# Performance work log

Hardware: AMD Instinct MI355X
Metric: run time of the kernel (lower is better)

## Reference

```python
import jax, jax.numpy as jnp
import numpy as np
from jax import lax

SEQ, BATCH, IN, HID, OUT = 28, 8192, 28, 128, 10


def _lstm_layer(x, W_ih, W_hh, b_ih, b_hh):
    # x: [T, B, in]; PyTorch gate order: i, f, g, o
    # precompute input projection once (keeps scan body memory-bound on h only)
    xproj = jnp.einsum('tbi,gi->tbg', x, W_ih) + b_ih + b_hh  # [T, B, 4H]
    H = W_hh.shape[1]
    B = x.shape[1]
    h0 = jnp.zeros((B, H), x.dtype)
    c0 = jnp.zeros((B, H), x.dtype)

    def step(carry, xp_t):
        h, c = carry
        gates = xp_t + h @ W_hh.T  # [B, 4H]
        i, f, g, o = jnp.split(gates, 4, axis=-1)
        i = jax.nn.sigmoid(i)
        f = jax.nn.sigmoid(f)
        g = jnp.tanh(g)
        o = jax.nn.sigmoid(o)
        c = f * c + i * g
        h = o * jnp.tanh(c)
        return (h, c), h

    _, ys = lax.scan(step, (h0, c0), xproj)
    return ys  # [T, B, H]


def setup_inputs() -> dict:
    key = jax.random.key(0)
    ks = jax.random.split(key, 11)
    s_in = 1.0 / np.sqrt(HID)
    u = lambda k, shape: jax.random.uniform(k, shape, jnp.float32, -s_in, s_in)
    return {
        'X': jax.random.normal(ks[0], (SEQ, BATCH, IN), jnp.float32),
        'W_ih0': u(ks[1], (4 * HID, IN)),
        'W_hh0': u(ks[2], (4 * HID, HID)),
        'b_ih0': u(ks[3], (4 * HID,)),
        'b_hh0': u(ks[4], (4 * HID,)),
        'W_ih1': u(ks[5], (4 * HID, HID)),
        'W_hh1': u(ks[6], (4 * HID, HID)),
        'b_ih1': u(ks[7], (4 * HID,)),
        'b_hh1': u(ks[8], (4 * HID,)),
        'W_lin': u(ks[9], (OUT, HID)),
        'b_lin': u(ks[10], (OUT,)),
    }


def reference(X, W_ih0, W_hh0, b_ih0, b_hh0, W_ih1, W_hh1, b_ih1, b_hh1, W_lin, b_lin):
    h1 = _lstm_layer(X, W_ih0, W_hh0, b_ih0, b_hh0)   # [T, B, 128]
    h2 = _lstm_layer(h1, W_ih1, W_hh1, b_ih1, b_hh1)  # [T, B, 128]
    pred = h2[-1] @ W_lin.T + b_lin                   # [B, 10]
    return pred
```

## Files before the change

kernel.cpp:

```cpp
#include <hip/hip_runtime.h>
#include <hip/hip_bf16.h>

#define SEQ   28
#define BATCH 8192
#define NIN   28
#define HID   128
#define NOUT  10

#define SCL_SIG  (-1.4426950408889634f)
#define SCL_TANH (2.8853900817779268f)

typedef __bf16 bf16_t;
typedef __bf16 bf16x8 __attribute__((ext_vector_type(8)));
typedef float  f32x4  __attribute__((ext_vector_type(4)));

__device__ __forceinline__ unsigned swz(unsigned row, unsigned byte_in_row) {
    return row * 256u + (byte_in_row ^ ((row & 7u) << 4));
}

__device__ __forceinline__ void barrier_lds() {
    asm volatile("s_waitcnt lgkmcnt(0)\n\ts_barrier" ::: "memory");
}

__global__ void pack_w_kernel(const float* __restrict__ Whh0, bf16_t* __restrict__ o0,
                              const float* __restrict__ Whh1, bf16_t* __restrict__ o1,
                              const float* __restrict__ Wih1, bf16_t* __restrict__ o2) {
    int idx = blockIdx.x * 256 + threadIdx.x;
    int mi = idx >> 16;
    int e  = idx & 65535;
    const float* W = (mi == 0) ? Whh0 : (mi == 1) ? Whh1 : Wih1;
    bf16_t*      o = (mi == 0) ? o0   : (mi == 1) ? o1   : o2;
    int j    = e & 7;
    int frag = e >> 3;
    int lane = frag & 63;
    int ksnt = frag >> 6;
    int nt = ksnt & 31, ks = ksnt >> 5;
    int gate = nt * 16 + (lane & 15);
    int k    = ks * 32 + ((lane >> 4) << 3) + j;
    float s  = ((gate >> 7) == 2) ? SCL_TANH : SCL_SIG;
    o[e] = (bf16_t)(W[gate * 128 + k] * s);
}

__device__ __forceinline__ bf16x8 load_x0(const float* __restrict__ X,
                                          int t, int rb, int m, int l15, int l4) {
    const float* base = X + ((size_t)(t * BATCH + rb + 16 * m + l15)) * NIN + l4 * 8;
    f32x4 lo = *(const f32x4*)base;
    f32x4 hi = {0.f, 0.f, 0.f, 0.f};
    if (l4 < 3) hi = *(const f32x4*)(base + 4);
    bf16x8 v;
    #pragma unroll
    for (int j = 0; j < 4; ++j) { v[j] = (bf16_t)lo[j]; v[4 + j] = (bf16_t)hi[j]; }
    return v;
}

template <int LAYER>
__device__ __forceinline__ void lstm_step(
    int t, int tload, int rb, int tid, int lane, int w, int l15, int l4,
    unsigned char* smem,
    const float* __restrict__ X, const bf16_t* __restrict__ h1r,
    bf16_t* __restrict__ h1w,
    bf16x8 (&whh)[4][4], bf16x8 (&wih)[4][4],
    float (&bias)[4], float (&c)[2][4],
    bf16x8 (&xc)[4][2], bf16x8 (&xl)[4][2])
{
    constexpr int KS = (LAYER == 0) ? 1 : 4;
    unsigned char* hb = smem + ((t & 1) << 13);
    unsigned char* hn = smem + ((~t & 1) << 13);

    bf16x8 ah[4][2];
    #pragma unroll
    for (int ks = 0; ks < 4; ++ks)
        #pragma unroll
        for (int m = 0; m < 2; ++m)
            ah[ks][m] = *(const bf16x8*)(hb + swz(16 * m + l15, (ks * 32 + l4 * 8) * 2));

    f32x4 acc[2][4];
    #pragma unroll
    for (int m = 0; m < 2; ++m)
        #pragma unroll
        for (int q = 0; q < 4; ++q) {
            f32x4 b = {bias[q], bias[q], bias[q], bias[q]};
            acc[m][q] = b;
        }

    #pragma unroll
    for (int m = 0; m < 2; ++m)
        #pragma unroll
        for (int q = 0; q < 4; ++q)
            #pragma unroll
            for (int ks = 0; ks < KS; ++ks)
                acc[m][q] = __builtin_amdgcn_mfma_f32_16x16x32_bf16(
                    xc[ks][m], wih[q][ks], acc[m][q], 0, 0, 0);

    if (tload < SEQ) {
        if constexpr (LAYER == 0) {
            #pragma unroll
            for (int m = 0; m < 2; ++m)
                xl[0][m] = load_x0(X, tload, rb, m, l15, l4);
        } else {
            #pragma unroll
            for (int ks = 0; ks < 4; ++ks)
                #pragma unroll
                for (int m = 0; m < 2; ++m)
                    xl[ks][m] = *(const bf16x8*)(h1r + ((size_t)(tload * BATCH + rb + 16 * m + l15)) * HID + ks * 32 + l4 * 8);
        }
    }

    #pragma unroll
    for (int m = 0; m < 2; ++m)
        #pragma unroll
        for (int q = 0; q < 4; ++q)
            #pragma unroll
            for (int ks = 0; ks < 4; ++ks)
                acc[m][q] = __builtin_amdgcn_mfma_f32_16x16x32_bf16(
                    ah[ks][m], whh[q][ks], acc[m][q], 0, 0, 0);

    #pragma unroll
    for (int m = 0; m < 2; ++m)
        #pragma unroll
        for (int r = 0; r < 4; ++r) {
            float Ei = __builtin_amdgcn_exp2f(acc[m][0][r]);
            float Ef = __builtin_amdgcn_exp2f(acc[m][1][r]);
            float Eg = __builtin_amdgcn_exp2f(acc[m][2][r]);
            float Eo = __builtin_amdgcn_exp2f(acc[m][3][r]);
            float ti = 1.0f + Ei, tf = 1.0f + Ef;
            float tg = 1.0f + Eg, to = 1.0f + Eo;
            float titg = ti * tg;
            float num  = fmaf(c[m][r], titg, tf * (tg - 2.0f));
            float cn   = num * __builtin_amdgcn_rcpf(tf * titg);
            c[m][r] = cn;
            float Ec = __builtin_amdgcn_exp2f(SCL_TANH * cn);
            float hv = (Ec - 1.0f) * __builtin_amdgcn_rcpf(to * (1.0f + Ec));
            *(bf16_t*)(hn + swz(16 * m + l4 * 4 + r, (16 * w + l15) * 2)) = (bf16_t)hv;
        }
    barrier_lds();

    if constexpr (LAYER == 0) {
        int row = tid >> 4, sc = tid & 15;
        f32x4 v = *(const f32x4*)(hn + swz(row, sc * 16));
        *(f32x4*)((unsigned char*)h1w + ((size_t)(t * BATCH + rb + row)) * 256 + sc * 16) = v;
    }
}

__global__ __launch_bounds__(512, 2)
void lstm_fused_kernel(const float* __restrict__ Wih0,
                       const float* __restrict__ bih0, const float* __restrict__ bhh0,
                       const float* __restrict__ bih1, const float* __restrict__ bhh1,
                       const float* __restrict__ X,
                       const bf16_t* __restrict__ whhp0,
                       const bf16_t* __restrict__ whhp1,
                       const bf16_t* __restrict__ wihp1,
                       bf16_t* __restrict__ h1,
                       const float* __restrict__ Wlin, const float* __restrict__ blin,
                       float* __restrict__ out)
{
    __shared__ unsigned char smem[16384] __attribute__((aligned(16)));

    const int tid  = threadIdx.x;
    const int lane = tid & 63;
    const int w    = tid >> 6;
    const int l15  = lane & 15;
    const int l4   = lane >> 4;
    const int rb   = blockIdx.x * 32;

    bf16x8 whh[4][4], wih[4][4];
    float  bias[4];
    float  c[2][4];
    bf16x8 xA[4][2], xB[4][2];

    #pragma unroll
    for (int q = 0; q < 4; ++q)
        #pragma unroll
        for (int ks = 0; ks < 4; ++ks)
            whh[q][ks] = *(const bf16x8*)(whhp0 + ((size_t)((ks * 32 + (w + 8 * q)) * 64 + lane)) * 8);
    #pragma unroll
    for (int q = 0; q < 4; ++q) {
        int gate = 16 * w + 128 * q + l15;
        float s = (q == 2) ? SCL_TANH : SCL_SIG;
        #pragma unroll
        for (int j = 0; j < 8; ++j) {
            int k = l4 * 8 + j;
            wih[q][0][j] = (k < NIN) ? (bf16_t)(Wih0[gate * NIN + k] * s) : (bf16_t)0.0f;
        }
        bias[q] = (bih0[gate] + bhh0[gate]) * s;
        c[0][q] = 0.f; c[1][q] = 0.f;
    }
    for (int i = tid * 16; i < 16384; i += 512 * 16) {
        f32x4 z = {0.f, 0.f, 0.f, 0.f};
        *(f32x4*)(smem + i) = z;
    }
    #pragma unroll
    for (int m = 0; m < 2; ++m) {
        xA[0][m] = load_x0(X, 0, rb, m, l15, l4);
        xB[0][m] = load_x0(X, 1, rb, m, l15, l4);
    }
    __syncthreads();

    for (int t = 0; t < SEQ; t += 2) {
        lstm_step<0>(t,     t + 2, rb, tid, lane, w, l15, l4, smem, X, nullptr, h1,
                     whh, wih, bias, c, xA, xA);
        lstm_step<0>(t + 1, t + 3, rb, tid, lane, w, l15, l4, smem, X, nullptr, h1,
                     whh, wih, bias, c, xB, xB);
    }

    __syncthreads();

    #pragma unroll
    for (int q = 0; q < 4; ++q) {
        #pragma unroll
        for (int ks = 0; ks < 4; ++ks) {
            whh[q][ks] = *(const bf16x8*)(whhp1 + ((size_t)((ks * 32 + (w + 8 * q)) * 64 + lane)) * 8);
            wih[q][ks] = *(const bf16x8*)(wihp1 + ((size_t)((ks * 32 + (w + 8 * q)) * 64 + lane)) * 8);
        }
        int gate = 16 * w + 128 * q + l15;
        float s = (q == 2) ? SCL_TANH : SCL_SIG;
        bias[q] = (bih1[gate] + bhh1[gate]) * s;
        c[0][q] = 0.f; c[1][q] = 0.f;
    }
    for (int i = tid * 16; i < 16384; i += 512 * 16) {
        f32x4 z = {0.f, 0.f, 0.f, 0.f};
        *(f32x4*)(smem + i) = z;
    }
    #pragma unroll
    for (int ks = 0; ks < 4; ++ks)
        #pragma unroll
        for (int m = 0; m < 2; ++m)
            xA[ks][m] = *(const bf16x8*)(h1 + ((size_t)(rb + 16 * m + l15)) * HID + ks * 32 + l4 * 8);
    __syncthreads();

    for (int t = 0; t < SEQ; ++t)
        lstm_step<1>(t, t + 1, rb, tid, lane, w, l15, l4, smem, nullptr, h1, nullptr,
                     whh, wih, bias, c, xA, xA);

    if (tid < 32 * NOUT) {
        int row = tid / NOUT, oc = tid % NOUT;
        const unsigned char* hf = smem;
        float s = blin[oc];
        #pragma unroll 8
        for (int k = 0; k < HID; ++k) {
            float h = (float)*(const bf16_t*)(hf + swz(row, k * 2));
            s += h * Wlin[oc * HID + k];
        }
        out[(size_t)(rb + row) * NOUT + oc] = s;
    }
}

extern "C" void kernel_launch(void* const* d_in, const int* in_sizes, int n_in,
                              void* d_out, int out_size, void* d_ws, size_t ws_size,
                              hipStream_t stream) {
    const float* X    = (const float*)d_in[0];
    const float* Wih0 = (const float*)d_in[1];
    const float* Whh0 = (const float*)d_in[2];
    const float* bih0 = (const float*)d_in[3];
    const float* bhh0 = (const float*)d_in[4];
    const float* Wih1 = (const float*)d_in[5];
    const float* Whh1 = (const float*)d_in[6];
    const float* bih1 = (const float*)d_in[7];
    const float* bhh1 = (const float*)d_in[8];
    const float* Wlin = (const float*)d_in[9];
    const float* blin = (const float*)d_in[10];
    float* out = (float*)d_out;

    unsigned char* ws = (unsigned char*)d_ws;
    bf16_t* h1    = (bf16_t*)(ws);
    bf16_t* whhp0 = (bf16_t*)(ws + 58720256);
    bf16_t* whhp1 = (bf16_t*)(ws + 58851328);
    bf16_t* wihp1 = (bf16_t*)(ws + 58982400);

    pack_w_kernel<<<dim3(768), dim3(256), 0, stream>>>(Whh0, whhp0, Whh1, whhp1, Wih1, wihp1);

    lstm_fused_kernel<<<dim3(256), dim3(512), 0, stream>>>(
        Wih0, bih0, bhh0, bih1, bhh1, X, whhp0, whhp1, wihp1, h1,
        Wlin, blin, out);
}
```

Before: 133.1 us.

## Software-pipeline LSTM steps: precompute next input projection during current step

Restructures each recurrent step so the input-projection MFMAs for the next timestep run after the current step's gate math, double-buffering accumulators across steps. The barrier moves to the start of each step and the h1 global writeback is deferred by one step, so the recurrent critical path holds only the h@W_hh MFMAs and the activations. The aim is to overlap independent input-projection work with the serial recurrence. The cost is more live registers (two accumulator sets), which may pressure occupancy at launch bounds (512,2).

```diff
diff --git a/kernel.cpp b/kernel.cpp
--- a/kernel.cpp
+++ b/kernel.cpp
@@ -54,75 +54,57 @@
 }
 
 template <int LAYER>
-__device__ __forceinline__ void lstm_step(
-    int t, int tload, int rb, int tid, int lane, int w, int l15, int l4,
+__device__ __forceinline__ void step_v2(
+    int t, int rb, int tid, int w, int l15, int l4,
     unsigned char* smem,
     const float* __restrict__ X, const bf16_t* __restrict__ h1r,
     bf16_t* __restrict__ h1w,
     bf16x8 (&whh)[4][4], bf16x8 (&wih)[4][4],
     float (&bias)[4], float (&c)[2][4],
-    bf16x8 (&xc)[4][2], bf16x8 (&xl)[4][2])
+    bf16x8 (&x)[4][2],
+    f32x4 (&accIn)[2][4], f32x4 (&accOut)[2][4])
 {
     constexpr int KS = (LAYER == 0) ? 1 : 4;
-    unsigned char* hb = smem + ((t & 1) << 13);
-    unsigned char* hn = smem + ((~t & 1) << 13);
-
-    bf16x8 ah[4][2];
-    #pragma unroll
-    for (int ks = 0; ks < 4; ++ks)
+    unsigned char* hb = smem + ((~t & 1) << 13);
+    unsigned char* hn = smem + ((t & 1) << 13);
+
+    barrier_lds();
+
+    if constexpr (LAYER == 0) {
+        if (t >= 1) {
+            int row = tid >> 4, sc = tid & 15;
+            f32x4 v = *(const f32x4*)(hb + swz(row, sc * 16));
+            *(f32x4*)((unsigned char*)h1w + ((size_t)((t - 1) * BATCH + rb + row)) * 256 + sc * 16) = v;
+        }
+    }
+
+    #pragma unroll
+    for (int kc = 0; kc < 2; ++kc) {
+        bf16x8 a0[2], a1[2];
+        #pragma unroll
+        for (int m = 0; m < 2; ++m) {
+            a0[m] = *(const bf16x8*)(hb + swz(16 * m + l15, ((2 * kc) * 32 + l4 * 8) * 2));
+            a1[m] = *(const bf16x8*)(hb + swz(16 * m + l15, ((2 * kc + 1) * 32 + l4 * 8) * 2));
+        }
         #pragma unroll
         for (int m = 0; m < 2; ++m)
-            ah[ks][m] = *(const bf16x8*)(hb + swz(16 * m + l15, (ks * 32 + l4 * 8) * 2));
-
-    f32x4 acc[2][4];
-    #pragma unroll
-    for (int m = 0; m < 2; ++m)
-        #pragma unroll
-        for (int q = 0; q < 4; ++q) {
-            f32x4 b = {bias[q], bias[q], bias[q], bias[q]};
-            acc[m][q] = b;
-        }
-
-    #pragma unroll
-    for (int m = 0; m < 2; ++m)
-        #pragma unroll
-        for (int q = 0; q < 4; ++q)
-            #pragma unroll
-            for (int ks = 0; ks < KS; ++ks)
-                acc[m][q] = __builtin_amdgcn_mfma_f32_16x16x32_bf16(
-                    xc[ks][m], wih[q][ks], acc[m][q], 0, 0, 0);
-
-    if (tload < SEQ) {
-        if constexpr (LAYER == 0) {
-            #pragma unroll
-            for (int m = 0; m < 2; ++m)
-                xl[0][m] = load_x0(X, tload, rb, m, l15, l4);
-        } else {
-            #pragma unroll
-            for (int ks = 0; ks < 4; ++ks)
-                #pragma unroll
-                for (int m = 0; m < 2; ++m)
-                    xl[ks][m] = *(const bf16x8*)(h1r + ((size_t)(tload * BATCH + rb + 16 * m + l15)) * HID + ks * 32 + l4 * 8);
-        }
-    }
-
-    #pragma unroll
-    for (int m = 0; m < 2; ++m)
-        #pragma unroll
-        for (int q = 0; q < 4; ++q)
-            #pragma unroll
-            for (int ks = 0; ks < 4; ++ks)
-                acc[m][q] = __builtin_amdgcn_mfma_f32_16x16x32_bf16(
-                    ah[ks][m], whh[q][ks], acc[m][q], 0, 0, 0);
-
-    #pragma unroll
-    for (int m = 0; m < 2; ++m)
+            #pragma unroll
+            for (int q = 0; q < 4; ++q) {
+                accIn[m][q] = __builtin_amdgcn_mfma_f32_16x16x32_bf16(
+                    a0[m], whh[q][2 * kc], accIn[m][q], 0, 0, 0);
+                accIn[m][q] = __builtin_amdgcn_mfma_f32_16x16x32_bf16(
+                    a1[m], whh[q][2 * kc + 1], accIn[m][q], 0, 0, 0);
+            }
+    }
+
+    #pragma unroll
+    for (int m = 0; m < 2; ++m) {
         #pragma unroll
         for (int r = 0; r < 4; ++r) {
-            float Ei = __builtin_amdgcn_exp2f(acc[m][0][r]);
-            float Ef = __builtin_amdgcn_exp2f(acc[m][1][r]);
-            float Eg = __builtin_amdgcn_exp2f(acc[m][2][r]);
-            float Eo = __builtin_amdgcn_exp2f(acc[m][3][r]);
+            float Ei = __builtin_amdgcn_exp2f(accIn[m][0][r]);
+            float Ef = __builtin_amdgcn_exp2f(accIn[m][1][r]);
+            float Eg = __builtin_amdgcn_exp2f(accIn[m][2][r]);
+            float Eo = __builtin_amdgcn_exp2f(accIn[m][3][r]);
             float ti = 1.0f + Ei, tf = 1.0f + Ef;
             float tg = 1.0f + Eg, to = 1.0f + Eo;
             float titg = ti * tg;
@@ -133,12 +115,29 @@
             float hv = (Ec - 1.0f) * __builtin_amdgcn_rcpf(to * (1.0f + Ec));
             *(bf16_t*)(hn + swz(16 * m + l4 * 4 + r, (16 * w + l15) * 2)) = (bf16_t)hv;
         }
-    barrier_lds();
-
-    if constexpr (LAYER == 0) {
-        int row = tid >> 4, sc = tid & 15;
-        f32x4 v = *(const f32x4*)(hn + swz(row, sc * 16));
-        *(f32x4*)((unsigned char*)h1w + ((size_t)(t * BATCH + rb + row)) * 256 + sc * 16) = v;
+        #pragma unroll
+        for (int q = 0; q < 4; ++q) {
+            f32x4 b = {bias[q], bias[q], bias[q], bias[q]};
+            accOut[m][q] = b;
+            #pragma unroll
+            for (int ks = 0; ks < KS; ++ks)
+                accOut[m][q] = __builtin_amdgcn_mfma_f32_16x16x32_bf16(
+                    x[ks][m], wih[q][ks], accOut[m][q], 0, 0, 0);
+        }
+    }
+
+    if (t + 2 < SEQ) {
+        if constexpr (LAYER == 0) {
+            #pragma unroll
+            for (int m = 0; m < 2; ++m)
+                x[0][m] = load_x0(X, t + 2, rb, m, l15, l4);
+        } else {
+            #pragma unroll
+            for (int ks = 0; ks < 4; ++ks)
+                #pragma unroll
+                for (int m = 0; m < 2; ++m)
+                    x[ks][m] = *(const bf16x8*)(h1r + ((size_t)((t + 2) * BATCH + rb + 16 * m + l15)) * HID + ks * 32 + l4 * 8);
+        }
     }
 }
 
@@ -166,7 +165,8 @@
     bf16x8 whh[4][4], wih[4][4];
     float  bias[4];
     float  c[2][4];
-    bf16x8 xA[4][2], xB[4][2];
+    bf16x8 x[4][2];
+    f32x4  accA[2][4], accB[2][4];
 
     #pragma unroll
     for (int q = 0; q < 4; ++q)
@@ -190,19 +190,33 @@
         *(f32x4*)(smem + i) = z;
     }
     #pragma unroll
-    for (int m = 0; m < 2; ++m) {
-        xA[0][m] = load_x0(X, 0, rb, m, l15, l4);
-        xB[0][m] = load_x0(X, 1, rb, m, l15, l4);
-    }
-    __syncthreads();
+    for (int m = 0; m < 2; ++m)
+        x[0][m] = load_x0(X, 0, rb, m, l15, l4);
+    #pragma unroll
+    for (int m = 0; m < 2; ++m)
+        #pragma unroll
+        for (int q = 0; q < 4; ++q) {
+            f32x4 b = {bias[q], bias[q], bias[q], bias[q]};
+            accA[m][q] = __builtin_amdgcn_mfma_f32_16x16x32_bf16(
+                x[0][m], wih[q][0], b, 0, 0, 0);
+        }
+    #pragma unroll
+    for (int m = 0; m < 2; ++m)
+        x[0][m] = load_x0(X, 1, rb, m, l15, l4);
 
     for (int t = 0; t < SEQ; t += 2) {
-        lstm_step<0>(t,     t + 2, rb, tid, lane, w, l15, l4, smem, X, nullptr, h1,
-                     whh, wih, bias, c, xA, xA);
-        lstm_step<0>(t + 1, t + 3, rb, tid, lane, w, l15, l4, smem, X, nullptr, h1,
-                     whh, wih, bias, c, xB, xB);
-    }
-
+        step_v2<0>(t,     rb, tid, w, l15, l4, smem, X, nullptr, h1,
+                   whh, wih, bias, c, x, accA, accB);
+        step_v2<0>(t + 1, rb, tid, w, l15, l4, smem, X, nullptr, h1,
+                   whh, wih, bias, c, x, accB, accA);
+    }
+
+    barrier_lds();
+    {
+        int row = tid >> 4, sc = tid & 15;
+        f32x4 v = *(const f32x4*)(smem + 8192 + swz(row, sc * 16));
+        *(f32x4*)((unsigned char*)h1 + ((size_t)(27 * BATCH + rb + row)) * 256 + sc * 16) = v;
+    }
     __syncthreads();
 
     #pragma unroll
@@ -225,16 +239,35 @@
     for (int ks = 0; ks < 4; ++ks)
         #pragma unroll
         for (int m = 0; m < 2; ++m)
-            xA[ks][m] = *(const bf16x8*)(h1 + ((size_t)(rb + 16 * m + l15)) * HID + ks * 32 + l4 * 8);
-    __syncthreads();
-
-    for (int t = 0; t < SEQ; ++t)
-        lstm_step<1>(t, t + 1, rb, tid, lane, w, l15, l4, smem, nullptr, h1, nullptr,
-                     whh, wih, bias, c, xA, xA);
+            x[ks][m] = *(const bf16x8*)(h1 + ((size_t)(rb + 16 * m + l15)) * HID + ks * 32 + l4 * 8);
+    #pragma unroll
+    for (int m = 0; m < 2; ++m)
+        #pragma unroll
+        for (int q = 0; q < 4; ++q) {
+            f32x4 b = {bias[q], bias[q], bias[q], bias[q]};
+            accA[m][q] = b;
+            #pragma unroll
+            for (int ks = 0; ks < 4; ++ks)
+                accA[m][q] = __builtin_amdgcn_mfma_f32_16x16x32_bf16(
+                    x[ks][m], wih[q][ks], accA[m][q], 0, 0, 0);
+        }
+    #pragma unroll
+    for (int ks = 0; ks < 4; ++ks)
+        #pragma unroll
+        for (int m = 0; m < 2; ++m)
+            x[ks][m] = *(const bf16x8*)(h1 + ((size_t)(BATCH + rb + 16 * m + l15)) * HID + ks * 32 + l4 * 8);
+
+    for (int t = 0; t < SEQ; t += 2) {
+        step_v2<1>(t,     rb, tid, w, l15, l4, smem, nullptr, h1, nullptr,
+                   whh, wih, bias, c, x, accA, accB);
+        step_v2<1>(t + 1, rb, tid, w, l15, l4, smem, nullptr, h1, nullptr,
+                   whh, wih, bias, c, x, accB, accA);
+    }
+    barrier_lds();
 
     if (tid < 32 * NOUT) {
         int row = tid / NOUT, oc = tid % NOUT;
-        const unsigned char* hf = smem;
+        const unsigned char* hf = smem + 8192;
         float s = blin[oc];
         #pragma unroll 8
         for (int k = 0; k < HID; ++k) {
```

After: 120.6 us. 1.1x faster.

## Software-pipeline LSTM steps by splitting batch tile into two interleaved halves

Applied to the files above, without the earlier changes.

The step is split into two half-steps over the two 16-row M tiles. The gate activations of one half are interleaved with the recurrent MFMAs of the other half, so transcendental math overlaps matrix work instead of running after it. The input projection for the next step is also issued early, and the h1 writeback is restructured per half. The cost is two barriers per timestep instead of one, plus more complex buffer parity logic with separate prologue and epilogue code.

```diff
diff --git a/kernel.cpp b/kernel.cpp
--- a/kernel.cpp
+++ b/kernel.cpp
@@ -13,6 +13,7 @@
 typedef __bf16 bf16_t;
 typedef __bf16 bf16x8 __attribute__((ext_vector_type(8)));
 typedef float  f32x4  __attribute__((ext_vector_type(4)));
+typedef float  f32x2  __attribute__((ext_vector_type(2)));
 
 __device__ __forceinline__ unsigned swz(unsigned row, unsigned byte_in_row) {
     return row * 256u + (byte_in_row ^ ((row & 7u) << 4));
@@ -53,92 +54,96 @@
     return v;
 }
 
-template <int LAYER>
-__device__ __forceinline__ void lstm_step(
-    int t, int tload, int rb, int tid, int lane, int w, int l15, int l4,
+__device__ __forceinline__ bf16_t act_elem(float z0, float z1, float z2, float z3,
+                                           float& cr) {
+    float Ei = __builtin_amdgcn_exp2f(z0);
+    float Ef = __builtin_amdgcn_exp2f(z1);
+    float Eg = __builtin_amdgcn_exp2f(z2);
+    float Eo = __builtin_amdgcn_exp2f(z3);
+    float ti = 1.0f + Ei, tf = 1.0f + Ef;
+    float tg = 1.0f + Eg, to = 1.0f + Eo;
+    float titg = ti * tg;
+    float cn = fmaf(cr, titg, tf * (tg - 2.0f)) * __builtin_amdgcn_rcpf(tf * titg);
+    cr = cn;
+    float Ec = __builtin_amdgcn_exp2f(SCL_TANH * cn);
+    float hv = (Ec - 1.0f) * __builtin_amdgcn_rcpf(to * (1.0f + Ec));
+    return (bf16_t)hv;
+}
+
+template <int LAYER, int MH, int PAR>
+__device__ __forceinline__ void half_step(
+    int th, int rb, int tid, int w, int l15, int l4,
     unsigned char* smem,
     const float* __restrict__ X, const bf16_t* __restrict__ h1r,
     bf16_t* __restrict__ h1w,
     bf16x8 (&whh)[4][4], bf16x8 (&wih)[4][4],
     float (&bias)[4], float (&c)[2][4],
-    bf16x8 (&xc)[4][2], bf16x8 (&xl)[4][2])
+    bf16x8 (&x)[4][2], f32x4 (&acc)[2][4])
 {
-    constexpr int KS = (LAYER == 0) ? 1 : 4;
-    unsigned char* hb = smem + ((t & 1) << 13);
-    unsigned char* hn = smem + ((~t & 1) << 13);
-
-    bf16x8 ah[4][2];
+    constexpr int MT  = 1 - MH;
+    constexpr int KS  = (LAYER == 0) ? 1 : 4;
+    constexpr int TBP = (MH == 0) ? (PAR ^ 1) : PAR;
+    unsigned char* bufR = smem + ((PAR ^ 1) << 13);
+    unsigned char* bufW = smem + (TBP << 13);
+    const int  tt    = (MH == 0) ? (th - 1) : th;
+    const bool do_tr = (MH == 1) || (th >= 1);
+
+    barrier_lds();
+
+    if constexpr (LAYER == 0) {
+        if (th >= 1) {
+            int row = MH * 16 + (tid >> 5);
+            int b8  = (tid & 31) * 8;
+            f32x2 v = *(const f32x2*)(bufR + swz(row, b8));
+            *(f32x2*)((unsigned char*)h1w + ((size_t)((th - 1) * BATCH + rb + row)) * 256 + b8) = v;
+        }
+    }
+
+    bf16x8 ah[4];
     #pragma unroll
     for (int ks = 0; ks < 4; ++ks)
-        #pragma unroll
-        for (int m = 0; m < 2; ++m)
-            ah[ks][m] = *(const bf16x8*)(hb + swz(16 * m + l15, (ks * 32 + l4 * 8) * 2));
-
-    f32x4 acc[2][4];
-    #pragma unroll
-    for (int m = 0; m < 2; ++m)
+        ah[ks] = *(const bf16x8*)(bufR + swz(16 * MH + l15, (ks * 32 + l4 * 8) * 2));
+
+    bf16_t hv[4];
+    if (do_tr)
+        hv[0] = act_elem(acc[MT][0][0], acc[MT][1][0], acc[MT][2][0], acc[MT][3][0], c[MT][0]);
+    #pragma unroll
+    for (int ks = 0; ks < 4; ++ks) {
+        #pragma unroll
+        for (int q = 0; q < 4; ++q)
+            acc[MH][q] = __builtin_amdgcn_mfma_f32_16x16x32_bf16(
+                ah[ks], whh[q][ks], acc[MH][q], 0, 0, 0);
+        if (ks < 3 && do_tr)
+            hv[ks + 1] = act_elem(acc[MT][0][ks + 1], acc[MT][1][ks + 1],
+                                  acc[MT][2][ks + 1], acc[MT][3][ks + 1], c[MT][ks + 1]);
+    }
+
+    if ((MH == 0) || (th < SEQ - 1)) {
         #pragma unroll
         for (int q = 0; q < 4; ++q) {
             f32x4 b = {bias[q], bias[q], bias[q], bias[q]};
-            acc[m][q] = b;
-        }
-
-    #pragma unroll
-    for (int m = 0; m < 2; ++m)
-        #pragma unroll
-        for (int q = 0; q < 4; ++q)
+            acc[MT][q] = b;
             #pragma unroll
             for (int ks = 0; ks < KS; ++ks)
-                acc[m][q] = __builtin_amdgcn_mfma_f32_16x16x32_bf16(
-                    xc[ks][m], wih[q][ks], acc[m][q], 0, 0, 0);
-
-    if (tload < SEQ) {
+                acc[MT][q] = __builtin_amdgcn_mfma_f32_16x16x32_bf16(
+                    x[ks][MT], wih[q][ks], acc[MT][q], 0, 0, 0);
+        }
+    }
+
+    if (do_tr) {
+        #pragma unroll
+        for (int r = 0; r < 4; ++r)
+            *(bf16_t*)(bufW + swz(16 * MT + l4 * 4 + r, (16 * w + l15) * 2)) = hv[r];
+    }
+
+    if (th < SEQ - 1 - MH) {
         if constexpr (LAYER == 0) {
-            #pragma unroll
-            for (int m = 0; m < 2; ++m)
-                xl[0][m] = load_x0(X, tload, rb, m, l15, l4);
+            x[0][MT] = load_x0(X, tt + 2, rb, MT, l15, l4);
         } else {
             #pragma unroll
             for (int ks = 0; ks < 4; ++ks)
-                #pragma unroll
-                for (int m = 0; m < 2; ++m)
-                    xl[ks][m] = *(const bf16x8*)(h1r + ((size_t)(tload * BATCH + rb + 16 * m + l15)) * HID + ks * 32 + l4 * 8);
-        }
-    }
-
-    #pragma unroll
-    for (int m = 0; m < 2; ++m)
-        #pragma unroll
-        for (int q = 0; q < 4; ++q)
-            #pragma unroll
-            for (int ks = 0; ks < 4; ++ks)
-                acc[m][q] = __builtin_amdgcn_mfma_f32_16x16x32_bf16(
-                    ah[ks][m], whh[q][ks], acc[m][q], 0, 0, 0);
-
-    #pragma unroll
-    for (int m = 0; m < 2; ++m)
-        #pragma unroll
-        for (int r = 0; r < 4; ++r) {
-            float Ei = __builtin_amdgcn_exp2f(acc[m][0][r]);
-            float Ef = __builtin_amdgcn_exp2f(acc[m][1][r]);
-            float Eg = __builtin_amdgcn_exp2f(acc[m][2][r]);
-            float Eo = __builtin_amdgcn_exp2f(acc[m][3][r]);
-            float ti = 1.0f + Ei, tf = 1.0f + Ef;
-            float tg = 1.0f + Eg, to = 1.0f + Eo;
-            float titg = ti * tg;
-            float num  = fmaf(c[m][r], titg, tf * (tg - 2.0f));
-            float cn   = num * __builtin_amdgcn_rcpf(tf * titg);
-            c[m][r] = cn;
-            float Ec = __builtin_amdgcn_exp2f(SCL_TANH * cn);
-            float hv = (Ec - 1.0f) * __builtin_amdgcn_rcpf(to * (1.0f + Ec));
-            *(bf16_t*)(hn + swz(16 * m + l4 * 4 + r, (16 * w + l15) * 2)) = (bf16_t)hv;
-        }
-    barrier_lds();
-
-    if constexpr (LAYER == 0) {
-        int row = tid >> 4, sc = tid & 15;
-        f32x4 v = *(const f32x4*)(hn + swz(row, sc * 16));
-        *(f32x4*)((unsigned char*)h1w + ((size_t)(t * BATCH + rb + row)) * 256 + sc * 16) = v;
+                x[ks][MT] = *(const bf16x8*)(h1r + ((size_t)((tt + 2) * BATCH + rb + 16 * MT + l15)) * HID + ks * 32 + l4 * 8);
+        }
     }
 }
 
@@ -166,7 +171,8 @@
     bf16x8 whh[4][4], wih[4][4];
     float  bias[4];
     float  c[2][4];
-    bf16x8 xA[4][2], xB[4][2];
+    bf16x8 x[4][2];
+    f32x4  acc[2][4];
 
     #pragma unroll
     for (int q = 0; q < 4; ++q)
@@ -189,20 +195,45 @@
         f32x4 z = {0.f, 0.f, 0.f, 0.f};
         *(f32x4*)(smem + i) = z;
     }
-    #pragma unroll
-    for (int m = 0; m < 2; ++m) {
-        xA[0][m] = load_x0(X, 0, rb, m, l15, l4);
-        xB[0][m] = load_x0(X, 1, rb, m, l15, l4);
-    }
-    __syncthreads();
-
-    for (int t = 0; t < SEQ; t += 2) {
-        lstm_step<0>(t,     t + 2, rb, tid, lane, w, l15, l4, smem, X, nullptr, h1,
-                     whh, wih, bias, c, xA, xA);
-        lstm_step<0>(t + 1, t + 3, rb, tid, lane, w, l15, l4, smem, X, nullptr, h1,
-                     whh, wih, bias, c, xB, xB);
-    }
-
+    x[0][0] = load_x0(X, 0, rb, 0, l15, l4);
+    x[0][1] = load_x0(X, 0, rb, 1, l15, l4);
+    #pragma unroll
+    for (int q = 0; q < 4; ++q) {
+        f32x4 b = {bias[q], bias[q], bias[q], bias[q]};
+        acc[0][q] = __builtin_amdgcn_mfma_f32_16x16x32_bf16(x[0][0], wih[q][0], b, 0, 0, 0);
+    }
+    x[0][0] = load_x0(X, 1, rb, 0, l15, l4);
+
+    for (int t2 = 0; t2 < SEQ; t2 += 2) {
+        half_step<0, 0, 0>(t2,     rb, tid, w, l15, l4, smem, X, nullptr, h1, whh, wih, bias, c, x, acc);
+        half_step<0, 1, 0>(t2,     rb, tid, w, l15, l4, smem, X, nullptr, h1, whh, wih, bias, c, x, acc);
+        half_step<0, 0, 1>(t2 + 1, rb, tid, w, l15, l4, smem, X, nullptr, h1, whh, wih, bias, c, x, acc);
+        half_step<0, 1, 1>(t2 + 1, rb, tid, w, l15, l4, smem, X, nullptr, h1, whh, wih, bias, c, x, acc);
+    }
+
+    barrier_lds();
+    {
+        int row = tid >> 5;
+        int b8  = (tid & 31) * 8;
+        f32x2 v = *(const f32x2*)(smem + 8192 + swz(row, b8));
+        *(f32x2*)((unsigned char*)h1 + ((size_t)(27 * BATCH + rb + row)) * 256 + b8) = v;
+    }
+    {
+        bf16_t hv[4];
+        #pragma unroll
+        for (int r = 0; r < 4; ++r)
+            hv[r] = act_elem(acc[1][0][r], acc[1][1][r], acc[1][2][r], acc[1][3][r], c[1][r]);
+        #pragma unroll
+        for (int r = 0; r < 4; ++r)
+            *(bf16_t*)(smem + 8192 + swz(16 + l4 * 4 + r, (16 * w + l15) * 2)) = hv[r];
+    }
+    barrier_lds();
+    {
+        int row = 16 + (tid >> 5);
+        int b8  = (tid & 31) * 8;
+        f32x2 v = *(const f32x2*)(smem + 8192 + swz(row, b8));
+        *(f32x2*)((unsigned char*)h1 + ((size_t)(27 * BATCH + rb + row)) * 256 + b8) = v;
+    }
     __syncthreads();
 
     #pragma unroll
@@ -222,19 +253,44 @@
         *(f32x4*)(smem + i) = z;
     }
     #pragma unroll
+    for (int ks = 0; ks < 4; ++ks) {
+        x[ks][0] = *(const bf16x8*)(h1 + ((size_t)(rb + l15)) * HID + ks * 32 + l4 * 8);
+        x[ks][1] = *(const bf16x8*)(h1 + ((size_t)(rb + 16 + l15)) * HID + ks * 32 + l4 * 8);
+    }
+    #pragma unroll
+    for (int q = 0; q < 4; ++q) {
+        f32x4 b = {bias[q], bias[q], bias[q], bias[q]};
+        acc[0][q] = b;
+        #pragma unroll
+        for (int ks = 0; ks < 4; ++ks)
+            acc[0][q] = __builtin_amdgcn_mfma_f32_16x16x32_bf16(x[ks][0], wih[q][ks], acc[0][q], 0, 0, 0);
+    }
+    #pragma unroll
     for (int ks = 0; ks < 4; ++ks)
-        #pragma unroll
-        for (int m = 0; m < 2; ++m)
-            xA[ks][m] = *(const bf16x8*)(h1 + ((size_t)(rb + 16 * m + l15)) * HID + ks * 32 + l4 * 8);
-    __syncthreads();
-
-    for (int t = 0; t < SEQ; ++t)
-        lstm_step<1>(t, t + 1, rb, tid, lane, w, l15, l4, smem, nullptr, h1, nullptr,
-                     whh, wih, bias, c, xA, xA);
+        x[ks][0] = *(const bf16x8*)(h1 + ((size_t)(BATCH + rb + l15)) * HID + ks * 32 + l4 * 8);
+
+    for (int t2 = 0; t2 < SEQ; t2 += 2) {
+        half_step<1, 0, 0>(t2,     rb, tid, w, l15, l4, smem, nullptr, h1, nullptr, whh, wih, bias, c, x, acc);
+        half_step<1, 1, 0>(t2,     rb, tid, w, l15, l4, smem, nullptr, h1, nullptr, whh, wih, bias, c, x, acc);
+        half_step<1, 0, 1>(t2 + 1, rb, tid, w, l15, l4, smem, nullptr, h1, nullptr, whh, wih, bias, c, x, acc);
+        half_step<1, 1, 1>(t2 + 1, rb, tid, w, l15, l4, smem, nullptr, h1, nullptr, whh, wih, bias, c, x, acc);
+    }
+
+    barrier_lds();
+    {
+        bf16_t hv[4];
+        #pragma unroll
+        for (int r = 0; r < 4; ++r)
+            hv[r] = act_elem(acc[1][0][r], acc[1][1][r], acc[1][2][r], acc[1][3][r], c[1][r]);
+        #pragma unroll
+        for (int r = 0; r < 4; ++r)
+            *(bf16_t*)(smem + 8192 + swz(16 + l4 * 4 + r, (16 * w + l15) * 2)) = hv[r];
+    }
+    barrier_lds();
 
     if (tid < 32 * NOUT) {
         int row = tid / NOUT, oc = tid % NOUT;
-        const unsigned char* hf = smem;
+        const unsigned char* hf = smem + 8192;
         float s = blin[oc];
         #pragma unroll 8
         for (int k = 0; k < HID; ++k) {
```

Result: faster. 123.0 us (-7.6%).

## Split gate work across 16 waves per 16-row tile with LDS exchange

Applied to the files above, without the earlier changes.

Each block now handles 16 batch rows with 1024 threads (16 waves) instead of 32 rows with 512 threads. Every wave computes two gate tiles, and the gate activations are swapped between wave halves through LDS so each thread finishes two cell elements. The h1 writeback is deferred by one step so it overlaps the next step. The goal is to halve the serial MFMA and elementwise work per wave in each recurrent step and to run 512 blocks for better occupancy, at the cost of an extra barrier and LDS round trip per step.

```diff
diff --git a/kernel.cpp b/kernel.cpp
--- a/kernel.cpp
+++ b/kernel.cpp
@@ -42,8 +42,8 @@
 }
 
 __device__ __forceinline__ bf16x8 load_x0(const float* __restrict__ X,
-                                          int t, int rb, int m, int l15, int l4) {
-    const float* base = X + ((size_t)(t * BATCH + rb + 16 * m + l15)) * NIN + l4 * 8;
+                                          int t, int rb, int l15, int l4) {
+    const float* base = X + ((size_t)(t * BATCH + rb + l15)) * NIN + l4 * 8;
     f32x4 lo = *(const f32x4*)base;
     f32x4 hi = {0.f, 0.f, 0.f, 0.f};
     if (l4 < 3) hi = *(const f32x4*)(base + 4);
@@ -53,96 +53,101 @@
     return v;
 }
 
-template <int LAYER>
-__device__ __forceinline__ void lstm_step(
-    int t, int tload, int rb, int tid, int lane, int w, int l15, int l4,
+__device__ __forceinline__ bf16_t finish_elem(float Ei, float Ef, float Eg, float Eo,
+                                              float& cr) {
+    float ti = 1.0f + Ei, tf = 1.0f + Ef;
+    float tg = 1.0f + Eg, to = 1.0f + Eo;
+    float titg = ti * tg;
+    float cn = fmaf(cr, titg, tf * (tg - 2.0f)) * __builtin_amdgcn_rcpf(tf * titg);
+    cr = cn;
+    float Ec = __builtin_amdgcn_exp2f(SCL_TANH * cn);
+    float hv = (Ec - 1.0f) * __builtin_amdgcn_rcpf(to * (1.0f + Ec));
+    return (bf16_t)hv;
+}
+
+template <int LAYER, int PAR>
+__device__ __forceinline__ void step16(
+    int t, int rb, int tid, int w, int l15, int l4,
     unsigned char* smem,
     const float* __restrict__ X, const bf16_t* __restrict__ h1r,
     bf16_t* __restrict__ h1w,
-    bf16x8 (&whh)[4][4], bf16x8 (&wih)[4][4],
-    float (&bias)[4], float (&c)[2][4],
-    bf16x8 (&xc)[4][2], bf16x8 (&xl)[4][2])
+    bf16x8 (&whh)[2][4], bf16x8 (&wih)[2][4],
+    float bias0, float bias1, float (&c)[2], bf16x8 (&x)[4])
 {
     constexpr int KS = (LAYER == 0) ? 1 : 4;
-    unsigned char* hb = smem + ((t & 1) << 13);
-    unsigned char* hn = smem + ((~t & 1) << 13);
-
-    bf16x8 ah[4][2];
+    unsigned char* hb   = smem + ((PAR ^ 1) << 12);
+    unsigned char* hn   = smem + (PAR << 12);
+    unsigned char* exch = smem + 8192;
+
+    barrier_lds();
+
+    if constexpr (LAYER == 0) {
+        if (t >= 1) {
+            int row = tid >> 6, b4 = (tid & 63) * 4;
+            float v = *(const float*)(hb + swz(row, b4));
+            *(float*)((unsigned char*)h1w + ((size_t)((t - 1) * BATCH + rb + row)) * 256 + b4) = v;
+        }
+    }
+
+    bf16x8 ah[4];
     #pragma unroll
     for (int ks = 0; ks < 4; ++ks)
-        #pragma unroll
-        for (int m = 0; m < 2; ++m)
-            ah[ks][m] = *(const bf16x8*)(hb + swz(16 * m + l15, (ks * 32 + l4 * 8) * 2));
-
-    f32x4 acc[2][4];
-    #pragma unroll
-    for (int m = 0; m < 2; ++m)
-        #pragma unroll
-        for (int q = 0; q < 4; ++q) {
-            f32x4 b = {bias[q], bias[q], bias[q], bias[q]};
-            acc[m][q] = b;
-        }
-
-    #pragma unroll
-    for (int m = 0; m < 2; ++m)
-        #pragma unroll
-        for (int q = 0; q < 4; ++q)
-            #pragma unroll
-            for (int ks = 0; ks < KS; ++ks)
-                acc[m][q] = __builtin_amdgcn_mfma_f32_16x16x32_bf16(
-                    xc[ks][m], wih[q][ks], acc[m][q], 0, 0, 0);
-
-    if (tload < SEQ) {
+        ah[ks] = *(const bf16x8*)(hb + swz(l15, (ks * 32 + l4 * 8) * 2));
+
+    f32x4 acc0 = {bias0, bias0, bias0, bias0};
+    f32x4 acc1 = {bias1, bias1, bias1, bias1};
+    #pragma unroll
+    for (int ks = 0; ks < 4; ++ks) {
+        acc0 = __builtin_amdgcn_mfma_f32_16x16x32_bf16(ah[ks], whh[0][ks], acc0, 0, 0, 0);
+        acc1 = __builtin_amdgcn_mfma_f32_16x16x32_bf16(ah[ks], whh[1][ks], acc1, 0, 0, 0);
+    }
+    #pragma unroll
+    for (int ks = 0; ks < KS; ++ks) {
+        acc0 = __builtin_amdgcn_mfma_f32_16x16x32_bf16(x[ks], wih[0][ks], acc0, 0, 0, 0);
+        acc1 = __builtin_amdgcn_mfma_f32_16x16x32_bf16(x[ks], wih[1][ks], acc1, 0, 0, 0);
+    }
+
+    f32x4 E0, E1;
+    #pragma unroll
+    for (int r = 0; r < 4; ++r) {
+        E0[r] = __builtin_amdgcn_exp2f(acc0[r]);
+        E1[r] = __builtin_amdgcn_exp2f(acc1[r]);
+    }
+
+    f32x4 snd;
+    if (w < 8) { snd[0] = E0[2]; snd[1] = E0[3]; snd[2] = E1[2]; snd[3] = E1[3]; }
+    else       { snd[0] = E0[0]; snd[1] = E0[1]; snd[2] = E1[0]; snd[3] = E1[1]; }
+    *(f32x4*)(exch + tid * 16) = snd;
+    barrier_lds();
+    f32x4 rcv = *(const f32x4*)(exch + (tid ^ 512) * 16);
+
+    int colb = ((w & 7) * 16 + l15) * 2;
+    if (w < 8) {
+        #pragma unroll
+        for (int j = 0; j < 2; ++j) {
+            bf16_t hv = finish_elem(E0[j], rcv[j], E1[j], rcv[2 + j], c[j]);
+            *(bf16_t*)(hn + swz(l4 * 4 + j, colb)) = hv;
+        }
+    } else {
+        #pragma unroll
+        for (int j = 0; j < 2; ++j) {
+            bf16_t hv = finish_elem(rcv[j], E0[2 + j], rcv[2 + j], E1[2 + j], c[j]);
+            *(bf16_t*)(hn + swz(l4 * 4 + 2 + j, colb)) = hv;
+        }
+    }
+
+    if (t + 1 < SEQ) {
         if constexpr (LAYER == 0) {
-            #pragma unroll
-            for (int m = 0; m < 2; ++m)
-                xl[0][m] = load_x0(X, tload, rb, m, l15, l4);
+            x[0] = load_x0(X, t + 1, rb, l15, l4);
         } else {
             #pragma unroll
             for (int ks = 0; ks < 4; ++ks)
-                #pragma unroll
-                for (int m = 0; m < 2; ++m)
-                    xl[ks][m] = *(const bf16x8*)(h1r + ((size_t)(tload * BATCH + rb + 16 * m + l15)) * HID + ks * 32 + l4 * 8);
-        }
-    }
-
-    #pragma unroll
-    for (int m = 0; m < 2; ++m)
-        #pragma unroll
-        for (int q = 0; q < 4; ++q)
-            #pragma unroll
-            for (int ks = 0; ks < 4; ++ks)
-                acc[m][q] = __builtin_amdgcn_mfma_f32_16x16x32_bf16(
-                    ah[ks][m], whh[q][ks], acc[m][q], 0, 0, 0);
-
-    #pragma unroll
-    for (int m = 0; m < 2; ++m)
-        #pragma unroll
-        for (int r = 0; r < 4; ++r) {
-            float Ei = __builtin_amdgcn_exp2f(acc[m][0][r]);
-            float Ef = __builtin_amdgcn_exp2f(acc[m][1][r]);
-            float Eg = __builtin_amdgcn_exp2f(acc[m][2][r]);
-            float Eo = __builtin_amdgcn_exp2f(acc[m][3][r]);
-            float ti = 1.0f + Ei, tf = 1.0f + Ef;
-            float tg = 1.0f + Eg, to = 1.0f + Eo;
-            float titg = ti * tg;
-            float num  = fmaf(c[m][r], titg, tf * (tg - 2.0f));
-            float cn   = num * __builtin_amdgcn_rcpf(tf * titg);
-            c[m][r] = cn;
-            float Ec = __builtin_amdgcn_exp2f(SCL_TANH * cn);
-            float hv = (Ec - 1.0f) * __builtin_amdgcn_rcpf(to * (1.0f + Ec));
-            *(bf16_t*)(hn + swz(16 * m + l4 * 4 + r, (16 * w + l15) * 2)) = (bf16_t)hv;
-        }
-    barrier_lds();
-
-    if constexpr (LAYER == 0) {
-        int row = tid >> 4, sc = tid & 15;
-        f32x4 v = *(const f32x4*)(hn + swz(row, sc * 16));
-        *(f32x4*)((unsigned char*)h1w + ((size_t)(t * BATCH + rb + row)) * 256 + sc * 16) = v;
-    }
-}
-
-__global__ __launch_bounds__(512, 2)
+                x[ks] = *(const bf16x8*)(h1r + ((size_t)((t + 1) * BATCH + rb + l15)) * HID + ks * 32 + l4 * 8);
+        }
+    }
+}
+
+__global__ __launch_bounds__(1024, 4)
 void lstm_fused_kernel(const float* __restrict__ Wih0,
                        const float* __restrict__ bih0, const float* __restrict__ bhh0,
                        const float* __restrict__ bih1, const float* __restrict__ bhh1,
@@ -154,87 +159,95 @@
                        const float* __restrict__ Wlin, const float* __restrict__ blin,
                        float* __restrict__ out)
 {
-    __shared__ unsigned char smem[16384] __attribute__((aligned(16)));
+    __shared__ unsigned char smem[24576] __attribute__((aligned(16)));
 
     const int tid  = threadIdx.x;
     const int lane = tid & 63;
     const int w    = tid >> 6;
     const int l15  = lane & 15;
     const int l4   = lane >> 4;
-    const int rb   = blockIdx.x * 32;
-
-    bf16x8 whh[4][4], wih[4][4];
-    float  bias[4];
-    float  c[2][4];
-    bf16x8 xA[4][2], xB[4][2];
-
-    #pragma unroll
-    for (int q = 0; q < 4; ++q)
+    const int rb   = blockIdx.x * 16;
+
+    bf16x8 whh[2][4], wih[2][4];
+    float  bias0, bias1;
+    float  c[2];
+    bf16x8 x[4];
+
+    #pragma unroll
+    for (int g = 0; g < 2; ++g)
         #pragma unroll
         for (int ks = 0; ks < 4; ++ks)
-            whh[q][ks] = *(const bf16x8*)(whhp0 + ((size_t)((ks * 32 + (w + 8 * q)) * 64 + lane)) * 8);
-    #pragma unroll
-    for (int q = 0; q < 4; ++q) {
-        int gate = 16 * w + 128 * q + l15;
-        float s = (q == 2) ? SCL_TANH : SCL_SIG;
+            whh[g][ks] = *(const bf16x8*)(whhp0 + ((size_t)((ks * 32 + (w + 16 * g)) * 64 + lane)) * 8);
+    #pragma unroll
+    for (int g = 0; g < 2; ++g) {
+        int tile = w + 16 * g;
+        int gate = 16 * tile + l15;
+        float s = ((tile >> 3) == 2) ? SCL_TANH : SCL_SIG;
         #pragma unroll
         for (int j = 0; j < 8; ++j) {
             int k = l4 * 8 + j;
-            wih[q][0][j] = (k < NIN) ? (bf16_t)(Wih0[gate * NIN + k] * s) : (bf16_t)0.0f;
-        }
-        bias[q] = (bih0[gate] + bhh0[gate]) * s;
-        c[0][q] = 0.f; c[1][q] = 0.f;
-    }
-    for (int i = tid * 16; i < 16384; i += 512 * 16) {
+            wih[g][0][j] = (k < NIN) ? (bf16_t)(Wih0[gate * NIN + k] * s) : (bf16_t)0.0f;
+        }
+    }
+    bias0 = (bih0[16 * w + l15] + bhh0[16 * w + l15]) * SCL_SIG;
+    {
+        int g1 = 16 * (w + 16) + l15;
+        bias1 = (bih0[g1] + bhh0[g1]) * ((w < 8) ? SCL_TANH : SCL_SIG);
+    }
+    c[0] = 0.f; c[1] = 0.f;
+    if (tid < 512) {
         f32x4 z = {0.f, 0.f, 0.f, 0.f};
-        *(f32x4*)(smem + i) = z;
-    }
-    #pragma unroll
-    for (int m = 0; m < 2; ++m) {
-        xA[0][m] = load_x0(X, 0, rb, m, l15, l4);
-        xB[0][m] = load_x0(X, 1, rb, m, l15, l4);
+        *(f32x4*)(smem + tid * 16) = z;
+    }
+    x[0] = load_x0(X, 0, rb, l15, l4);
+
+    for (int t = 0; t < SEQ; t += 2) {
+        step16<0, 0>(t,     rb, tid, w, l15, l4, smem, X, nullptr, h1,
+                     whh, wih, bias0, bias1, c, x);
+        step16<0, 1>(t + 1, rb, tid, w, l15, l4, smem, X, nullptr, h1,
+                     whh, wih, bias0, bias1, c, x);
+    }
+
+    barrier_lds();
+    {
+        int row = tid >> 6, b4 = (tid & 63) * 4;
+        float v = *(const float*)(smem + 4096 + swz(row, b4));
+        *(float*)((unsigned char*)h1 + ((size_t)(27 * BATCH + rb + row)) * 256 + b4) = v;
     }
     __syncthreads();
 
+    #pragma unroll
+    for (int g = 0; g < 2; ++g)
+        #pragma unroll
+        for (int ks = 0; ks < 4; ++ks) {
+            whh[g][ks] = *(const bf16x8*)(whhp1 + ((size_t)((ks * 32 + (w + 16 * g)) * 64 + lane)) * 8);
+            wih[g][ks] = *(const bf16x8*)(wihp1 + ((size_t)((ks * 32 + (w + 16 * g)) * 64 + lane)) * 8);
+        }
+    bias0 = (bih1[16 * w + l15] + bhh1[16 * w + l15]) * SCL_SIG;
+    {
+        int g1 = 16 * (w + 16) + l15;
+        bias1 = (bih1[g1] + bhh1[g1]) * ((w < 8) ? SCL_TANH : SCL_SIG);
+    }
+    c[0] = 0.f; c[1] = 0.f;
+    if (tid < 512) {
+        f32x4 z = {0.f, 0.f, 0.f, 0.f};
+        *(f32x4*)(smem + tid * 16) = z;
+    }
+    #pragma unroll
+    for (int ks = 0; ks < 4; ++ks)
+        x[ks] = *(const bf16x8*)(h1 + ((size_t)(rb + l15)) * HID + ks * 32 + l4 * 8);
+
     for (int t = 0; t < SEQ; t += 2) {
-        lstm_step<0>(t,     t + 2, rb, tid, lane, w, l15, l4, smem, X, nullptr, h1,
-                     whh, wih, bias, c, xA, xA);
-        lstm_step<0>(t + 1, t + 3, rb, tid, lane, w, l15, l4, smem, X, nullptr, h1,
-                     whh, wih, bias, c, xB, xB);
-    }
-
-    __syncthreads();
-
-    #pragma unroll
-    for (int q = 0; q < 4; ++q) {
-        #pragma unroll
-        for (int ks = 0; ks < 4; ++ks) {
-            whh[q][ks] = *(const bf16x8*)(whhp1 + ((size_t)((ks * 32 + (w + 8 * q)) * 64 + lane)) * 8);
-            wih[q][ks] = *(const bf16x8*)(wihp1 + ((size_t)((ks * 32 + (w + 8 * q)) * 64 + lane)) * 8);
-        }
-        int gate = 16 * w + 128 * q + l15;
-        float s = (q == 2) ? SCL_TANH : SCL_SIG;
-        bias[q] = (bih1[gate] + bhh1[gate]) * s;
-        c[0][q] = 0.f; c[1][q] = 0.f;
-    }
-    for (int i = tid * 16; i < 16384; i += 512 * 16) {
-        f32x4 z = {0.f, 0.f, 0.f, 0.f};
-        *(f32x4*)(smem + i) = z;
-    }
-    #pragma unroll
-    for (int ks = 0; ks < 4; ++ks)
-        #pragma unroll
-        for (int m = 0; m < 2; ++m)
-            xA[ks][m] = *(const bf16x8*)(h1 + ((size_t)(rb + 16 * m + l15)) * HID + ks * 32 + l4 * 8);
-    __syncthreads();
-
-    for (int t = 0; t < SEQ; ++t)
-        lstm_step<1>(t, t + 1, rb, tid, lane, w, l15, l4, smem, nullptr, h1, nullptr,
-                     whh, wih, bias, c, xA, xA);
-
-    if (tid < 32 * NOUT) {
+        step16<1, 0>(t,     rb, tid, w, l15, l4, smem, nullptr, h1, nullptr,
+                     whh, wih, bias0, bias1, c, x);
+        step16<1, 1>(t + 1, rb, tid, w, l15, l4, smem, nullptr, h1, nullptr,
+                     whh, wih, bias0, bias1, c, x);
+    }
+    barrier_lds();
+
+    if (tid < 16 * NOUT) {
         int row = tid / NOUT, oc = tid % NOUT;
-        const unsigned char* hf = smem;
+        const unsigned char* hf = smem + 4096;
         float s = blin[oc];
         #pragma unroll 8
         for (int k = 0; k < HID; ++k) {
@@ -269,7 +282,7 @@
 
     pack_w_kernel<<<dim3(768), dim3(256), 0, stream>>>(Whh0, whhp0, Whh1, whhp1, Wih1, wihp1);
 
-    lstm_fused_kernel<<<dim3(256), dim3(512), 0, stream>>>(
+    lstm_fused_kernel<<<dim3(512), dim3(1024), 0, stream>>>(
         Wih0, bih0, bhh0, bih1, bhh1, X, whhp0, whhp1, wihp1, h1,
         Wlin, blin, out);
 }
```

After: 213.4 us. +60.3%, slower.
